# Kernel optimization log

Measured on AMD Instinct MI355X. Metric: run time of the kernel, lower is better.

The kernel has to match this reference:

```python
import jax, jax.numpy as jnp
import numpy as np

B, T, D, P = 8, 2048, 768, 1024


def setup_inputs() -> dict:
    key = jax.random.key(0)
    kx, kp = jax.random.split(key)
    x = jax.random.normal(kx, (B, T, D), dtype=jnp.float32)
    prototypes = jax.random.normal(kp, (P, D), dtype=jnp.float32)
    return {"x": x, "prototypes": prototypes}


def reference(x, prototypes):
    # sum((x[...,None,:] - p)**2, -1) without the [B,T,P,D] intermediate)
    x_sq = jnp.sum(x * x, axis=-1, keepdims=True)          # [B,T,1]
    p_sq = jnp.sum(prototypes * prototypes, axis=-1)        # [P]
    cross = jnp.einsum("btd,pd->btp", x, prototypes)       # [B,T,P]
    distances = x_sq + p_sq[None, None, :] - 2.0 * cross    # [B,T,P]
    return distances, prototypes
```

## Files before the change

### kernel.cpp

```cpp
#include <hip/hip_runtime.h>
#include <hip/hip_bf16.h>
#include <stdint.h>

#define M_ROWS 16384
#define N_COLS 1024
#define K_DIM  768
#define NKT    12

typedef __attribute__((ext_vector_type(8))) short bf16x8;
typedef __attribute__((ext_vector_type(4))) float f32x4;

__device__ __forceinline__ void async_copy16(void* lds, const void* g) {
  __builtin_amdgcn_global_load_lds(
      (const __attribute__((address_space(1))) unsigned int*)g,
      (__attribute__((address_space(3))) unsigned int*)lds,
      16, 0, 0);
}

__device__ __forceinline__ unsigned short f2bf(float f) {
  __hip_bfloat16 h = __float2bfloat16(f);
  return *reinterpret_cast<unsigned short*>(&h);
}

__global__ void prep_all(const float* __restrict__ x,
                         const float* __restrict__ p,
                         unsigned short* __restrict__ xb,
                         unsigned short* __restrict__ pbu,
                         float* __restrict__ xsq,
                         float* __restrict__ psq,
                         float* __restrict__ proto_out) {
  const int b = blockIdx.x;
  const int wid = threadIdx.x >> 6;
  const int lane = threadIdx.x & 63;
  const float* src;
  unsigned short* dst;
  float* sq;
  float* cp;
  int row;
  if (b < M_ROWS / 4) {
    row = b * 4 + wid;
    src = x; dst = xb; sq = xsq; cp = nullptr;
  } else {
    row = (b - M_ROWS / 4) * 4 + wid;
    src = p; dst = pbu; sq = psq; cp = proto_out;
  }
  const float4* r = (const float4*)(src + (size_t)row * K_DIM);
  ushort4* rb = (ushort4*)(dst + (size_t)row * K_DIM);
  float4* cpv = cp ? (float4*)(cp + (size_t)row * K_DIM) : nullptr;
  float acc = 0.f;
#pragma unroll
  for (int i = 0; i < 3; ++i) {
    float4 v = r[i * 64 + lane];
    acc += v.x * v.x + v.y * v.y + v.z * v.z + v.w * v.w;
    ushort4 u;
    u.x = f2bf(v.x); u.y = f2bf(v.y); u.z = f2bf(v.z); u.w = f2bf(v.w);
    rb[i * 64 + lane] = u;
    if (cpv) cpv[i * 64 + lane] = v;
  }
#pragma unroll
  for (int off = 32; off; off >>= 1) acc += __shfl_down(acc, off);
  if (lane == 0) sq[row] = acc;
}

__device__ __forceinline__ bf16x8 ldsfrag(const char* tile, int row, int slot) {
  return *(const bf16x8*)(tile + row * 128 + (((slot ^ (row & 7)) << 4)));
}

__global__ __launch_bounds__(512, 4) void dist_gemm(
    const __hip_bfloat16* __restrict__ xb,
    const __hip_bfloat16* __restrict__ pb,
    const float* __restrict__ xsq,
    const float* __restrict__ psq,
    float* __restrict__ out) {
  __shared__ char lds[2][2][16384];

  const int flat = blockIdx.x;
  const int xcd = flat & 7;
  const int local = flat >> 3;
  const int bm = xcd * 16 + (local >> 3);
  const int bn = local & 7;

  const int tid = threadIdx.x;
  const int wave = tid >> 6;
  const int lane = tid & 63;
  const int wm = wave >> 2;
  const int wn = wave & 3;
  const int rl = lane & 15;
  const int kq = lane >> 4;

  f32x4 acc[4][2] = {};
  bf16x8 af[4][2], bfr[2][2];

  const __hip_bfloat16* Abase = xb + (size_t)(bm * 128) * K_DIM;
  const __hip_bfloat16* Bbase = pb + (size_t)(bn * 128) * K_DIM;

  int gofs[2];
#pragma unroll
  for (int c = 0; c < 2; ++c) {
    const int row = c * 64 + (tid >> 3);
    const int g = (tid & 7) ^ (row & 7);
    gofs[c] = row * K_DIM + g * 8;
  }

#define STAGE(buf, ktile)                                                   \
  do {                                                                      \
    _Pragma("unroll") for (int c = 0; c < 2; ++c) {                         \
      const int lofs = (c * 512 + tid) * 16;                                \
      async_copy16(&lds[buf][0][0] + lofs, Abase + gofs[c] + (ktile) * 64); \
      async_copy16(&lds[buf][1][0] + lofs, Bbase + gofs[c] + (ktile) * 64); \
    }                                                                       \
  } while (0)

  STAGE(0, 0);
  asm volatile("s_waitcnt vmcnt(0)" ::: "memory");
  asm volatile("s_barrier" ::: "memory");

  for (int kt = 0; kt < NKT; ++kt) {
    const int cur = kt & 1;
    if (kt + 1 < NKT) STAGE(cur ^ 1, kt + 1);

    const char* At = &lds[cur][0][0];
    const char* Bt = &lds[cur][1][0];
#pragma unroll
    for (int mi = 0; mi < 4; ++mi)
#pragma unroll
      for (int kk = 0; kk < 2; ++kk)
        af[mi][kk] = ldsfrag(At, wm * 64 + mi * 16 + rl, kk * 4 + kq);
#pragma unroll
    for (int ni = 0; ni < 2; ++ni)
#pragma unroll
      for (int kk = 0; kk < 2; ++kk)
        bfr[ni][kk] = ldsfrag(Bt, wn * 32 + ni * 16 + rl, kk * 4 + kq);

    __builtin_amdgcn_s_setprio(1);
#pragma unroll
    for (int mi = 0; mi < 4; ++mi)
#pragma unroll
      for (int ni = 0; ni < 2; ++ni)
#pragma unroll
        for (int kk = 0; kk < 2; ++kk)
          acc[mi][ni] = __builtin_amdgcn_mfma_f32_16x16x32_bf16(
              af[mi][kk], bfr[ni][kk], acc[mi][ni], 0, 0, 0);
    __builtin_amdgcn_s_setprio(0);

    asm volatile("s_waitcnt vmcnt(0)" ::: "memory");
    asm volatile("s_barrier" ::: "memory");
  }
#undef STAGE

  const int c0 = bn * 128 + wn * 32;
  const int r0 = bm * 128 + wm * 64;
#pragma unroll
  for (int mi = 0; mi < 4; ++mi) {
#pragma unroll
    for (int ni = 0; ni < 2; ++ni) {
      const int col = c0 + ni * 16 + rl;
      const float ps = psq[col];
#pragma unroll
      for (int r = 0; r < 4; ++r) {
        const int row = r0 + mi * 16 + kq * 4 + r;
        out[(size_t)row * N_COLS + col] = xsq[row] + ps - 2.0f * acc[mi][ni][r];
      }
    }
  }
}

extern "C" void kernel_launch(void* const* d_in, const int* in_sizes, int n_in,
                              void* d_out, int out_size, void* d_ws, size_t ws_size,
                              hipStream_t stream) {
  const float* x = (const float*)d_in[0];
  const float* p = (const float*)d_in[1];
  float* out = (float*)d_out;
  char* ws = (char*)d_ws;

  float* xsq = (float*)ws;
  float* psq = (float*)(ws + 65536);
  unsigned short* xb = (unsigned short*)(ws + 69632);
  unsigned short* pbu = xb + (size_t)M_ROWS * K_DIM;
  float* proto_out = out + (size_t)M_ROWS * N_COLS;

  prep_all<<<M_ROWS / 4 + N_COLS / 4, 256, 0, stream>>>(x, p, xb, pbu, xsq,
                                                        psq, proto_out);

  dist_gemm<<<1024, 512, 0, stream>>>((const __hip_bfloat16*)xb,
                                      (const __hip_bfloat16*)pbu,
                                      xsq, psq, out);
}
```

Baseline: 47.34 us.

## Enlarge GEMM tile to 256x256 with interleaved ping-pong LDS pipeline

Switches the distance GEMM from 128x128 tiles with a simple double buffer to 256x256 tiles per 512-thread block, using 128KB of LDS split into half-tiles. Loads of A/B halves are interleaved with LDS fragment reads and MFMA groups under barriers, in a hand-scheduled ping-pong. The goal is to raise arithmetic intensity and cut global/LDS traffic per FLOP. The cost is higher register pressure (128 accumulator floats), a grid of only 256 blocks with lower occupancy, and many extra barriers.

```diff
diff --git a/kernel.cpp b/kernel.cpp
--- a/kernel.cpp
+++ b/kernel.cpp
@@ -5,7 +5,7 @@
 #define M_ROWS 16384
 #define N_COLS 1024
 #define K_DIM  768
-#define NKT    12
+#define NIT    6
 
 typedef __attribute__((ext_vector_type(8))) short bf16x8;
 typedef __attribute__((ext_vector_type(4))) float f32x4;
@@ -62,23 +62,19 @@
   if (lane == 0) sq[row] = acc;
 }
 
-__device__ __forceinline__ bf16x8 ldsfrag(const char* tile, int row, int slot) {
-  return *(const bf16x8*)(tile + row * 128 + (((slot ^ (row & 7)) << 4)));
-}
-
-__global__ __launch_bounds__(512, 4) void dist_gemm(
+__global__ __launch_bounds__(512, 2) void dist_gemm(
     const __hip_bfloat16* __restrict__ xb,
     const __hip_bfloat16* __restrict__ pb,
     const float* __restrict__ xsq,
     const float* __restrict__ psq,
     float* __restrict__ out) {
-  __shared__ char lds[2][2][16384];
+  __shared__ char L[131072];
 
   const int flat = blockIdx.x;
   const int xcd = flat & 7;
   const int local = flat >> 3;
-  const int bm = xcd * 16 + (local >> 3);
-  const int bn = local & 7;
+  const int bm = xcd * 8 + (local >> 2);
+  const int bn = local & 3;
 
   const int tid = threadIdx.x;
   const int wave = tid >> 6;
@@ -88,78 +84,140 @@
   const int rl = lane & 15;
   const int kq = lane >> 4;
 
-  f32x4 acc[4][2] = {};
-  bf16x8 af[4][2], bfr[2][2];
-
-  const __hip_bfloat16* Abase = xb + (size_t)(bm * 128) * K_DIM;
-  const __hip_bfloat16* Bbase = pb + (size_t)(bn * 128) * K_DIM;
-
-  int gofs[2];
-#pragma unroll
-  for (int c = 0; c < 2; ++c) {
-    const int row = c * 64 + (tid >> 3);
-    const int g = (tid & 7) ^ (row & 7);
-    gofs[c] = row * K_DIM + g * 8;
-  }
-
-#define STAGE(buf, ktile)                                                   \
-  do {                                                                      \
-    _Pragma("unroll") for (int c = 0; c < 2; ++c) {                         \
-      const int lofs = (c * 512 + tid) * 16;                                \
-      async_copy16(&lds[buf][0][0] + lofs, Abase + gofs[c] + (ktile) * 64); \
-      async_copy16(&lds[buf][1][0] + lofs, Bbase + gofs[c] + (ktile) * 64); \
-    }                                                                       \
-  } while (0)
-
-  STAGE(0, 0);
-  asm volatile("s_waitcnt vmcnt(0)" ::: "memory");
-  asm volatile("s_barrier" ::: "memory");
-
-  for (int kt = 0; kt < NKT; ++kt) {
-    const int cur = kt & 1;
-    if (kt + 1 < NKT) STAGE(cur ^ 1, kt + 1);
-
-    const char* At = &lds[cur][0][0];
-    const char* Bt = &lds[cur][1][0];
-#pragma unroll
-    for (int mi = 0; mi < 4; ++mi)
-#pragma unroll
-      for (int kk = 0; kk < 2; ++kk)
-        af[mi][kk] = ldsfrag(At, wm * 64 + mi * 16 + rl, kk * 4 + kq);
-#pragma unroll
-    for (int ni = 0; ni < 2; ++ni)
-#pragma unroll
-      for (int kk = 0; kk < 2; ++kk)
-        bfr[ni][kk] = ldsfrag(Bt, wn * 32 + ni * 16 + rl, kk * 4 + kq);
-
-    __builtin_amdgcn_s_setprio(1);
-#pragma unroll
-    for (int mi = 0; mi < 4; ++mi)
-#pragma unroll
-      for (int ni = 0; ni < 2; ++ni)
-#pragma unroll
-        for (int kk = 0; kk < 2; ++kk)
-          acc[mi][ni] = __builtin_amdgcn_mfma_f32_16x16x32_bf16(
-              af[mi][kk], bfr[ni][kk], acc[mi][ni], 0, 0, 0);
-    __builtin_amdgcn_s_setprio(0);
-
-    asm volatile("s_waitcnt vmcnt(0)" ::: "memory");
-    asm volatile("s_barrier" ::: "memory");
-  }
-#undef STAGE
-
-  const int c0 = bn * 128 + wn * 32;
-  const int r0 = bm * 128 + wm * 64;
-#pragma unroll
-  for (int mi = 0; mi < 4; ++mi) {
-#pragma unroll
-    for (int ni = 0; ni < 2; ++ni) {
-      const int col = c0 + ni * 16 + rl;
+  f32x4 acc[8][4] = {};
+  bf16x8 af[4][2];
+  bf16x8 bfr[4][2];
+
+  const __hip_bfloat16* Abase = xb + (size_t)(bm * 256) * K_DIM;
+  const __hip_bfloat16* Bbase = pb + (size_t)(bn * 256) * K_DIM;
+
+  const int rih = tid >> 3;
+  const int g8 = ((tid & 7) ^ (rih & 7)) * 8;
+
+#define STG(buf_, op_, h_, base_, kt_)                                       \
+  do {                                                                       \
+    _Pragma("unroll") for (int c = 0; c < 2; ++c)                            \
+        async_copy16(L + (buf_) * 65536 + (op_) * 32768 + (h_) * 16384 +     \
+                         (c * 512 + tid) * 16,                               \
+                     (base_) + (size_t)((h_) * 128 + c * 64 + rih) * K_DIM + \
+                         (kt_) * 64 + g8);                                   \
+  } while (0)
+
+#define RD_A(buf_, mh_)                                                      \
+  do {                                                                       \
+    _Pragma("unroll") for (int mi2 = 0; mi2 < 4; ++mi2)                      \
+        _Pragma("unroll") for (int kk = 0; kk < 2; ++kk) {                   \
+      const int r_ = (mh_) * 64 + mi2 * 16 + rl;                             \
+      af[mi2][kk] = *(const bf16x8*)(L + (buf_) * 65536 + wm * 16384 +       \
+                                     r_ * 128 +                              \
+                                     (((kk * 4 + kq) ^ (r_ & 7)) << 4));     \
+    }                                                                        \
+  } while (0)
+
+#define RD_B(buf_, nh_)                                                      \
+  do {                                                                       \
+    _Pragma("unroll") for (int ni2 = 0; ni2 < 2; ++ni2)                      \
+        _Pragma("unroll") for (int kk = 0; kk < 2; ++kk) {                   \
+      const int r_ = (wn & 1) * 64 + ((nh_) * 2 + ni2) * 16 + rl;            \
+      bfr[(nh_) * 2 + ni2][kk] =                                             \
+          *(const bf16x8*)(L + (buf_) * 65536 + 32768 + (wn >> 1) * 16384 +  \
+                           r_ * 128 + (((kk * 4 + kq) ^ (r_ & 7)) << 4));    \
+    }                                                                        \
+  } while (0)
+
+#define MMA(mh_, nh_)                                                        \
+  do {                                                                       \
+    __builtin_amdgcn_s_setprio(1);                                           \
+    _Pragma("unroll") for (int mi2 = 0; mi2 < 4; ++mi2)                      \
+        _Pragma("unroll") for (int ni2 = 0; ni2 < 2; ++ni2)                  \
+            _Pragma("unroll") for (int kk = 0; kk < 2; ++kk)                 \
+        acc[(mh_) * 4 + mi2][(nh_) * 2 + ni2] =                              \
+            __builtin_amdgcn_mfma_f32_16x16x32_bf16(                         \
+                af[mi2][kk], bfr[(nh_) * 2 + ni2][kk],                       \
+                acc[(mh_) * 4 + mi2][(nh_) * 2 + ni2], 0, 0, 0);             \
+    __builtin_amdgcn_s_setprio(0);                                           \
+  } while (0)
+
+#define BAR()   asm volatile("s_barrier" ::: "memory")
+#define LGKM0() asm volatile("s_waitcnt lgkmcnt(0)" ::: "memory")
+
+  STG(0, 0, 0, Abase, 0);
+  STG(0, 0, 1, Abase, 0);
+  STG(0, 1, 0, Bbase, 0);
+  STG(0, 1, 1, Bbase, 0);
+  STG(1, 1, 0, Bbase, 1);
+  STG(1, 1, 1, Bbase, 1);
+  asm volatile("s_waitcnt vmcnt(4)" ::: "memory");
+  BAR();
+
+  for (int i = 0; i < NIT; ++i) {
+    const int T1 = 2 * i + 1;
+    const int T2n = 2 * i + 2;
+    const int T3n = 2 * i + 3;
+    const bool pf = (i < NIT - 1);
+
+    RD_A(0, 0); RD_B(0, 0);
+    STG(1, 0, 0, Abase, T1);
+    BAR(); LGKM0();
+    MMA(0, 0);
+    BAR();
+    RD_B(0, 1);
+    STG(1, 0, 1, Abase, T1);
+    BAR(); LGKM0();
+    MMA(0, 1);
+    BAR();
+    RD_A(0, 1);
+    if (pf) STG(0, 1, 0, Bbase, T2n);
+    BAR(); LGKM0();
+    MMA(1, 0);
+    BAR();
+    if (pf) STG(0, 1, 1, Bbase, T2n);
+    BAR();
+    MMA(1, 1);
+    if (pf) asm volatile("s_waitcnt vmcnt(4)" ::: "memory");
+    else    asm volatile("s_waitcnt vmcnt(0)" ::: "memory");
+    BAR();
+
+    RD_A(1, 0); RD_B(1, 0);
+    if (pf) STG(0, 0, 0, Abase, T2n);
+    BAR(); LGKM0();
+    MMA(0, 0);
+    BAR();
+    RD_B(1, 1);
+    if (pf) STG(0, 0, 1, Abase, T2n);
+    BAR(); LGKM0();
+    MMA(0, 1);
+    BAR();
+    RD_A(1, 1);
+    if (pf) STG(1, 1, 0, Bbase, T3n);
+    BAR(); LGKM0();
+    MMA(1, 0);
+    BAR();
+    if (pf) STG(1, 1, 1, Bbase, T3n);
+    BAR();
+    MMA(1, 1);
+    if (pf) asm volatile("s_waitcnt vmcnt(4)" ::: "memory");
+    BAR();
+  }
+#undef STG
+#undef RD_A
+#undef RD_B
+#undef MMA
+#undef BAR
+#undef LGKM0
+
+  const int c0 = bn * 256 + wn * 64;
+  const int r0 = bm * 256 + wm * 128;
+#pragma unroll
+  for (int mf = 0; mf < 8; ++mf) {
+#pragma unroll
+    for (int nf = 0; nf < 4; ++nf) {
+      const int col = c0 + nf * 16 + rl;
       const float ps = psq[col];
 #pragma unroll
       for (int r = 0; r < 4; ++r) {
-        const int row = r0 + mi * 16 + kq * 4 + r;
-        out[(size_t)row * N_COLS + col] = xsq[row] + ps - 2.0f * acc[mi][ni][r];
+        const int row = r0 + mf * 16 + kq * 4 + r;
+        out[(size_t)row * N_COLS + col] = xsq[row] + ps - 2.0f * acc[mf][nf][r];
       }
     }
   }
@@ -182,7 +240,7 @@
   prep_all<<<M_ROWS / 4 + N_COLS / 4, 256, 0, stream>>>(x, p, xb, pbu, xsq,
                                                         psq, proto_out);
 
-  dist_gemm<<<1024, 512, 0, stream>>>((const __hip_bfloat16*)xb,
-                                      (const __hip_bfloat16*)pbu,
-                                      xsq, psq, out);
-}
+  dist_gemm<<<256, 512, 0, stream>>>((const __hip_bfloat16*)xb,
+                                     (const __hip_bfloat16*)pbu,
+                                     xsq, psq, out);
+}
```

Measured after the change: 48.89 us. 3.3% more time.
